# Optimization experiments

Measured on AMD Instinct MI355X. Metric: run time of the kernel, lower is better.

The kernel has to match this reference:

```python
import jax, jax.numpy as jnp
import numpy as np

L, D = 1024, 256
NDIR, NL = 6, 2
H, P, N, K = 8, 64, 32, 4          # nheads, headdim, d_state, d_conv
DI = 2 * D                          # d_inner = expand * d_model
DIN = 2 * DI + 2 * N + H            # in_proj output width (z, xBC, dt)
CONV_DIM = DI + 2 * N               # channels going through depthwise conv
ORDERS = [(0, 1, 2), (0, 2, 1), (1, 0, 2), (1, 2, 0), (2, 0, 1), (2, 1, 0)]  # XYT,XTY,YXT,YTX,TXY,TYX


def setup_inputs() -> dict:
    ks = jax.random.split(jax.random.key(0), 12)
    s = 0.02
    f32 = jnp.float32
    return {
        "vectors": jax.random.normal(ks[0], (L, D), f32),
        "event_coords": jax.random.randint(ks[1], (L, 4), 0, 64, jnp.int32),
        "ln_g": jnp.ones((NDIR, NL, D), f32),
        "ln_b": jnp.zeros((NDIR, NL, D), f32),
        "Win": jax.random.normal(ks[2], (NDIR, NL, D, DIN), f32) * s,
        "conv_w": jax.random.normal(ks[3], (NDIR, NL, CONV_DIM, K), f32) * s,
        "conv_b": jnp.zeros((NDIR, NL, CONV_DIM), f32),
        "dt_bias": jax.random.normal(ks[4], (NDIR, NL, H), f32) * 0.5,
        "A_log": jnp.log(jax.random.uniform(ks[5], (NDIR, NL, H), f32, 1.0, 16.0)),
        "Dp": jnp.ones((NDIR, NL, H), f32),
        "rms_g": jnp.ones((NDIR, NL, DI), f32),
        "Wout": jax.random.normal(ks[6], (NDIR, NL, DI, D), f32) * s,
        "fuse_ln_g": jnp.ones((NDIR * D,), f32),
        "fuse_ln_b": jnp.zeros((NDIR * D,), f32),
        "fuse_W": jax.random.normal(ks[7], (NDIR * D, D), f32) * s,
        "fuse_b": jnp.zeros((D,), f32),
    }


def _layernorm(x, g, b, eps=1e-5):
    mu = jnp.mean(x, -1, keepdims=True)
    var = jnp.mean((x - mu) ** 2, -1, keepdims=True)
    return (x - mu) * jax.lax.rsqrt(var + eps) * g + b


def _causal_dwconv(x, w, b):
    # x: [Bt,L,C]; w: [C,K]. Torch depthwise conv1d with padding K-1, truncated to L.
    k = w.shape[1]
    Lx = x.shape[1]
    xp = jnp.pad(x, ((0, 0), (k - 1, 0), (0, 0)))
    return sum(xp[:, j:j + Lx, :] * w[:, j] for j in range(k)) + b


def _mamba2(x, Win, conv_w, conv_b, dt_bias, A_log, Dp, rms_g, Wout):
    # x: [Bt,L,D] -> [Bt,L,D]. Mamba2 with ngroups=1, rmsnorm gating, no proj biases.
    Bt, Lx, _ = x.shape
    zxbcdt = x @ Win
    z = zxbcdt[..., :DI]
    xBC = zxbcdt[..., DI:DI + CONV_DIM]
    dt = jax.nn.softplus(zxbcdt[..., -H:] + dt_bias)              # [Bt,L,H]
    xBC = jax.nn.silu(_causal_dwconv(xBC, conv_w, conv_b))
    xs = xBC[..., :DI].reshape(Bt, Lx, H, P)                      # [Bt,L,H,P]
    Bm = xBC[..., DI:DI + N]                                      # [Bt,L,N]
    Cm = xBC[..., DI + N:]                                        # [Bt,L,N]
    dA = jnp.exp(dt * (-jnp.exp(A_log)))                          # [Bt,L,H]
    dBx = jnp.einsum('blh,bln,blhp->blhpn', dt, Bm, xs)

    def step(h, inp):
        dA_t, dBx_t, C_t = inp
        h = dA_t[:, :, None, None] * h + dBx_t                    # [Bt,H,P,N]
        return h, jnp.einsum('bhpn,bn->bhp', h, C_t)

    h0 = jnp.zeros((Bt, H, P, N), x.dtype)
    _, ys = jax.lax.scan(step, h0, (dA.transpose(1, 0, 2),
                                    dBx.transpose(1, 0, 2, 3, 4),
                                    Cm.transpose(1, 0, 2)))
    y = ys.transpose(1, 0, 2, 3) + Dp[:, None] * xs               # [Bt,L,H,P]
    u = y.reshape(Bt, Lx, DI) * jax.nn.silu(z)                    # gated RMSNorm
    u = u * jax.lax.rsqrt(jnp.mean(u * u, -1, keepdims=True) + 1e-5) * rms_g
    return u @ Wout


def _forward(vectors, event_coords, ln_g, ln_b, Win, conv_w, conv_b, dt_bias,
             A_log, Dp, rms_g, Wout, fuse_ln_g, fuse_ln_b, fuse_W, fuse_b):
    v = vectors[None]                                             # [1,L,D]
    outs = []
    for i, axes in enumerate(ORDERS):
        idx = jnp.lexsort(tuple(event_coords[:, a] for a in reversed(axes)))
        x = v[:, idx, :]
        for l in range(NL):
            x = x + _mamba2(_layernorm(x, ln_g[i, l], ln_b[i, l]),
                            Win[i, l], conv_w[i, l], conv_b[i, l], dt_bias[i, l],
                            A_log[i, l], Dp[i, l], rms_g[i, l], Wout[i, l])
        outs.append(x[:, jnp.argsort(idx), :])                    # scatter back
    md = jnp.concatenate(outs, -1)                                # [1,L,6D]
    f = _layernorm(md, fuse_ln_g, fuse_ln_b) @ fuse_W + fuse_b
    return jax.nn.gelu(f, approximate=False)[0]                   # [L,D]


def reference(vectors, event_coords, ln_g, ln_b, Win, conv_w, conv_b, dt_bias,
              A_log, Dp, rms_g, Wout, fuse_ln_g, fuse_ln_b, fuse_W, fuse_b):
    return _forward(vectors, event_coords, ln_g, ln_b, Win, conv_w, conv_b, dt_bias,
                    A_log, Dp, rms_g, Wout, fuse_ln_g, fuse_ln_b, fuse_W, fuse_b)
```

## Files before the change

kernel.cpp:

```cpp
#include <hip/hip_runtime.h>
#include <hip/hip_bf16.h>
#include <cstddef>

#define LL 1024
#define DD0 256
#define NDIR 6
#define NL 2
#define HH 8
#define PP 64
#define NN 32
#define KK 4
#define DI 512
#define DIN 1096
#define CONV_DIM 576

#define QC 32
#define NC 32
#define NCSH 5

__constant__ int c_ord[6][3] = {{0,1,2},{0,2,1},{1,0,2},{1,2,0},{2,0,1},{2,1,0}};

typedef __attribute__((ext_vector_type(8))) short bf16x8;
typedef __attribute__((ext_vector_type(4))) float f32x4;

__device__ inline float blockReduceSum256(float v) {
    __shared__ float sred[4];
#pragma unroll
    for (int off = 1; off < 64; off <<= 1) v += __shfl_xor(v, off);
    int lane = threadIdx.x & 63, w = threadIdx.x >> 6;
    __syncthreads();
    if (lane == 0) sred[w] = v;
    __syncthreads();
    return sred[0] + sred[1] + sred[2] + sred[3];
}

__device__ inline float siluf(float x) { return x / (1.f + expf(-x)); }

__device__ inline unsigned short bf16_rn(float x) {
    unsigned u = __float_as_uint(x);
    unsigned r = (u + 0x7fffu + ((u >> 16) & 1u)) >> 16;
    return (unsigned short)r;
}
__device__ inline float bf16_to_f(unsigned short h) {
    return __uint_as_float(((unsigned)h) << 16);
}

__global__ __launch_bounds__(1024)
void sort_kernel(const int* __restrict__ coords, int* __restrict__ perm, int* __restrict__ rank) {
    int q = blockIdx.x, d = blockIdx.y;
    int tid = threadIdx.x;
    __shared__ unsigned keys[LL];
    __shared__ unsigned short part[256][5];
    int a0 = c_ord[d][0], a1 = c_ord[d][1], a2 = c_ord[d][2];
    {
        unsigned c0 = (unsigned)coords[tid*4 + a0];
        unsigned c1 = (unsigned)coords[tid*4 + a1];
        unsigned c2 = (unsigned)coords[tid*4 + a2];
        keys[tid] = (c0 << 22) | (c1 << 16) | (c2 << 10) | (unsigned)tid;
    }
    __syncthreads();
    int il = tid >> 2, jq = tid & 3;
    int i = q*256 + il;
    unsigned ki = keys[i];
    int r = 0;
    int j0 = jq*256;
#pragma unroll 8
    for (int j = j0; j < j0 + 256; ++j) r += (keys[j] < ki) ? 1 : 0;
    part[il][jq] = (unsigned short)r;
    __syncthreads();
    if (tid < 256) {
        int i2 = q*256 + tid;
        int rr = part[tid][0] + part[tid][1] + part[tid][2] + part[tid][3];
        perm[d*LL + rr] = i2;
        rank[d*LL + i2] = rr;
    }
}

__global__ __launch_bounds__(256)
void gather_ln(const float* __restrict__ vectors, const int* __restrict__ perm,
               float* __restrict__ x, unsigned short* __restrict__ Yh,
               unsigned short* __restrict__ Yl,
               const float* __restrict__ g, const float* __restrict__ b) {
    int t = blockIdx.x, d = blockIdx.y, c = threadIdx.x;
    int src = perm[d*LL + t];
    float xv = vectors[(size_t)src*DD0 + c];
    x[((size_t)d*LL + t)*DD0 + c] = xv;
    float s = blockReduceSum256(xv);
    float s2 = blockReduceSum256(xv*xv);
    float mu = s / DD0;
    float var = s2 / DD0 - mu*mu;
    float inv = rsqrtf(var + 1e-5f);
    const float* gr = g + (size_t)d*NL*DD0;
    const float* br = b + (size_t)d*NL*DD0;
    float yv = (xv - mu) * inv * gr[c] + br[c];
    unsigned short h = bf16_rn(yv);
    Yh[((size_t)d*LL + t)*DD0 + c] = h;
    Yl[((size_t)d*LL + t)*DD0 + c] = bf16_rn(yv - bf16_to_f(h));
}

__global__ __launch_bounds__(256)
void ln_split(const float* __restrict__ X, unsigned short* __restrict__ Yh,
              unsigned short* __restrict__ Yl,
              const float* __restrict__ g, const float* __restrict__ b,
              int dd, int rowsPerDir, int gstride) {
    int t = blockIdx.x, d = blockIdx.y;
    const float* xr = X + ((size_t)d*rowsPerDir + t)*dd;
    unsigned short* yh = Yh + ((size_t)d*rowsPerDir + t)*dd;
    unsigned short* yl = Yl + ((size_t)d*rowsPerDir + t)*dd;
    const float* gr = g + (size_t)d*gstride;
    const float* br = b + (size_t)d*gstride;
    float v[6];
    float s = 0.f, s2 = 0.f;
    int cnt = 0;
    for (int c = threadIdx.x; c < dd; c += 256) {
        float xv = xr[c];
        v[cnt++] = xv;
        s += xv; s2 += xv*xv;
    }
    float tot = blockReduceSum256(s);
    float tot2 = blockReduceSum256(s2);
    float mu = tot / dd;
    float var = tot2 / dd - mu*mu;
    float inv = rsqrtf(var + 1e-5f);
    cnt = 0;
    for (int c = threadIdx.x; c < dd; c += 256) {
        float yv = (v[cnt++] - mu) * inv * gr[c] + br[c];
        unsigned short h = bf16_rn(yv);
        yh[c] = h;
        yl[c] = bf16_rn(yv - bf16_to_f(h));
    }
}

__global__ __launch_bounds__(256)
void ln_concat(const float* __restrict__ x, const int* __restrict__ rank,
               unsigned short* __restrict__ Yh, unsigned short* __restrict__ Yl,
               const float* __restrict__ g, const float* __restrict__ b) {
    int t = blockIdx.x, tid = threadIdx.x;
    float v[NDIR];
    float s = 0.f, s2 = 0.f;
#pragma unroll
    for (int d = 0; d < NDIR; ++d) {
        int r = rank[d*LL + t];
        float xv = x[((size_t)d*LL + r)*DD0 + tid];
        v[d] = xv;
        s += xv; s2 += xv*xv;
    }
    float tot = blockReduceSum256(s);
    float tot2 = blockReduceSum256(s2);
    const int dd = NDIR*DD0;
    float mu = tot / dd;
    float var = tot2 / dd - mu*mu;
    float inv = rsqrtf(var + 1e-5f);
#pragma unroll
    for (int d = 0; d < NDIR; ++d) {
        int c = d*DD0 + tid;
        float yv = (v[d] - mu) * inv * g[c] + b[c];
        unsigned short h = bf16_rn(yv);
        Yh[(size_t)t*dd + c] = h;
        Yl[(size_t)t*dd + c] = bf16_rn(yv - bf16_to_f(h));
    }
}

__global__ __launch_bounds__(256)
void tsplit_kernel(const float* __restrict__ W, unsigned short* __restrict__ Th,
                   unsigned short* __restrict__ Tl, int Kd, int Nd) {
    __shared__ float tile[32][33];
    int j0 = blockIdx.x * 32;
    int i0 = blockIdx.y * 32;
    int c = threadIdx.x & 31, r8 = threadIdx.x >> 5;
    const float* Wz = W + (size_t)blockIdx.z * Kd * Nd;
    unsigned short* Thz = Th + (size_t)blockIdx.z * Nd * Kd;
    unsigned short* Tlz = Tl + (size_t)blockIdx.z * Nd * Kd;
#pragma unroll
    for (int s = 0; s < 4; ++s) {
        int i = i0 + r8 + s*8;
        tile[r8 + s*8][c] = (i < Kd && (j0 + c) < Nd) ? Wz[(size_t)i*Nd + j0 + c] : 0.f;
    }
    __syncthreads();
#pragma unroll
    for (int s = 0; s < 4; ++s) {
        int j = j0 + r8 + s*8;
        int i = i0 + c;
        if (j < Nd && i < Kd) {
            float xv = tile[c][r8 + s*8];
            unsigned short h = bf16_rn(xv);
            Thz[(size_t)j*Kd + i] = h;
            Tlz[(size_t)j*Kd + i] = bf16_rn(xv - bf16_to_f(h));
        }
    }
}

template<int MODE, int BM>
__global__ __launch_bounds__(256)
void mfma_gemm(const unsigned short* __restrict__ Ahg, const unsigned short* __restrict__ Alg,
               const unsigned short* __restrict__ Bhg, const unsigned short* __restrict__ Blg,
               float* __restrict__ Cg, int N, int K,
               size_t sA, size_t sB, size_t sC, const float* __restrict__ bias,
               int ksplit) {
    constexpr int MF = BM / 32;
    __shared__ unsigned short AhS[2][BM][40];
    __shared__ unsigned short AlS[2][BM][40];
    __shared__ unsigned short BhS[2][64][40];
    __shared__ unsigned short BlS[2][64][40];
    const unsigned short* Azh = Ahg + (MODE == 3 ? 0 : (size_t)blockIdx.z * sA);
    const unsigned short* Azl = Alg + (MODE == 3 ? 0 : (size_t)blockIdx.z * sA);
    const unsigned short* Bzh = Bhg + (MODE == 3 ? 0 : (size_t)blockIdx.z * sB);
    const unsigned short* Bzl = Blg + (MODE == 3 ? 0 : (size_t)blockIdx.z * sB);
    float* Cz = Cg + (size_t)blockIdx.z * sC;
    int row0 = blockIdx.y * BM;
    int col0 = blockIdx.x * 64;
    int tid = threadIdx.x;
    int lane = tid & 63, wid = tid >> 6;
    int mbase = (wid >> 1) * (BM/2), nbase = (wid & 1) * 32;
    int lr = lane & 15, lk = (lane >> 4) * 8;

    int ar0 = tid >> 2;
    int ar1 = 64 + (tid >> 2);
    int ac  = (tid & 3) * 8;
    int brow = tid >> 2;
    int bc8 = (tid & 3) * 8;
    bool bvalid = (col0 + brow) < N;
    const uint4 z4 = {0u,0u,0u,0u};

    f32x4 acc[MF][2];
#pragma unroll
    for (int m = 0; m < MF; ++m)
#pragma unroll
        for (int n = 0; n < 2; ++n) acc[m][n] = (f32x4){0.f, 0.f, 0.f, 0.f};

    uint4 s0a0, s0a1, s0l0, s0l1, s0bh, s0bl;
    uint4 s1a0, s1a1, s1l0, s1l1, s1bh, s1bl;

#define LOAD_TILE(Ra0,Ra1,Rl0,Rl1,Rbh,Rbl,kt) do {                          \
        size_t ka = (size_t)(kt) * 32;                                       \
        size_t g0 = (size_t)(row0 + ar0)*K + ka + ac;                        \
        Ra0 = *(const uint4*)(Azh + g0);                                     \
        Rl0 = *(const uint4*)(Azl + g0);                                     \
        if (BM == 128) {                                                     \
            size_t g1 = (size_t)(row0 + ar1)*K + ka + ac;                    \
            Ra1 = *(const uint4*)(Azh + g1);                                 \
            Rl1 = *(const uint4*)(Azl + g1);                                 \
        }                                                                    \
        if (bvalid) {                                                        \
            size_t gb = (size_t)(col0 + brow)*K + ka + bc8;                  \
            Rbh = *(const uint4*)(Bzh + gb);                                 \
            Rbl = *(const uint4*)(Bzl + gb);                                 \
        } else { Rbh = z4; Rbl = z4; }                                       \
    } while (0)

#define WRITE_TILE(buf,Ra0,Ra1,Rl0,Rl1,Rbh,Rbl) do {                         \
        *(uint4*)&AhS[buf][ar0][ac] = Ra0;                                   \
        *(uint4*)&AlS[buf][ar0][ac] = Rl0;                                   \
        if (BM == 128) {                                                     \
            *(uint4*)&AhS[buf][ar1 & (BM-1)][ac] = Ra1;                      \
            *(uint4*)&AlS[buf][ar1 & (BM-1)][ac] = Rl1;                      \
        }                                                                    \
        *(uint4*)&BhS[buf][brow][bc8] = Rbh;                                 \
        *(uint4*)&BlS[buf][brow][bc8] = Rbl;                                 \
    } while (0)

#define COMPUTE(buf) do {                                                    \
        bf16x8 afh[MF], afl[MF], bfh[2], bfl[2];                             \
        _Pragma("unroll")                                                    \
        for (int mf = 0; mf < MF; ++mf) {                                    \
            afh[mf] = *(const bf16x8*)&AhS[buf][mbase + mf*16 + lr][lk];     \
            afl[mf] = *(const bf16x8*)&AlS[buf][mbase + mf*16 + lr][lk];     \
        }                                                                    \
        _Pragma("unroll")                                                    \
        for (int nf = 0; nf < 2; ++nf) {                                     \
            bfh[nf] = *(const bf16x8*)&BhS[buf][nbase + nf*16 + lr][lk];     \
            bfl[nf] = *(const bf16x8*)&BlS[buf][nbase + nf*16 + lr][lk];     \
        }                                                                    \
        _Pragma("unroll")                                                    \
        for (int mf = 0; mf < MF; ++mf)                                      \
            _Pragma("unroll")                                                \
            for (int nf = 0; nf < 2; ++nf) {                                 \
                acc[mf][nf] = __builtin_amdgcn_mfma_f32_16x16x32_bf16(afh[mf], bfh[nf], acc[mf][nf], 0, 0, 0); \
                acc[mf][nf] = __builtin_amdgcn_mfma_f32_16x16x32_bf16(afh[mf], bfl[nf], acc[mf][nf], 0, 0, 0); \
                acc[mf][nf] = __builtin_amdgcn_mfma_f32_16x16x32_bf16(afl[mf], bfh[nf], acc[mf][nf], 0, 0, 0); \
            }                                                                \
    } while (0)

    int nt, kt0;
    if (MODE == 3) { nt = ksplit; kt0 = (int)blockIdx.z * ksplit; }
    else           { nt = K >> 5; kt0 = 0; }

    LOAD_TILE(s0a0, s0a1, s0l0, s0l1, s0bh, s0bl, kt0 + 0);
    LOAD_TILE(s1a0, s1a1, s1l0, s1l1, s1bh, s1bl, kt0 + 1);
    WRITE_TILE(0, s0a0, s0a1, s0l0, s0l1, s0bh, s0bl);
    __syncthreads();

    for (int t = 0; t < nt; t += 2) {
        if (t + 2 < nt) LOAD_TILE(s0a0, s0a1, s0l0, s0l1, s0bh, s0bl, kt0 + t + 2);
        COMPUTE(0);
        WRITE_TILE(1, s1a0, s1a1, s1l0, s1l1, s1bh, s1bl);
        __syncthreads();
        if (t + 3 < nt) LOAD_TILE(s1a0, s1a1, s1l0, s1l1, s1bh, s1bl, kt0 + t + 3);
        COMPUTE(1);
        if (t + 2 < nt) WRITE_TILE(0, s0a0, s0a1, s0l0, s0l1, s0bh, s0bl);
        __syncthreads();
    }

#undef LOAD_TILE
#undef WRITE_TILE
#undef COMPUTE

    int crb = (lane >> 4) * 4;
    int cco = lane & 15;
#pragma unroll
    for (int mf = 0; mf < MF; ++mf) {
#pragma unroll
        for (int nf = 0; nf < 2; ++nf) {
            int col = col0 + nbase + nf*16 + cco;
            if (col < N) {
#pragma unroll
                for (int r = 0; r < 4; ++r) {
                    int row = row0 + mbase + mf*16 + crb + r;
                    size_t o = (size_t)row*N + col;
                    float vv = acc[mf][nf][r];
                    if (MODE == 0 || MODE == 3) Cz[o] = vv;
                    else if (MODE == 1) Cz[o] += vv;
                    else {
                        vv += bias[col];
                        Cz[o] = 0.5f * vv * (1.f + erff(vv * 0.70710678118654752f));
                    }
                }
            }
        }
    }
}

__global__ __launch_bounds__(256)
void reduce_gelu(const float* __restrict__ pbuf, const float* __restrict__ bias,
                 float* __restrict__ out) {
    int t = blockIdx.x, c = threadIdx.x;
    size_t o = (size_t)t*DD0 + c;
    const size_t st = (size_t)LL*DD0;
    float v = pbuf[o] + pbuf[o + st] + pbuf[o + 2*st] + pbuf[o + 3*st] + bias[c];
    out[o] = 0.5f * v * (1.f + erff(v * 0.70710678118654752f));
}

__global__ __launch_bounds__(256)
void conv_scan1(const float* __restrict__ zx, const float* __restrict__ conv_w,
                const float* __restrict__ conv_b, const float* __restrict__ dt_bias,
                const float* __restrict__ A_log, const float* __restrict__ Dp,
                float* __restrict__ ys, float* __restrict__ Cbuf,
                float* __restrict__ cstate, float* __restrict__ cumdec, int layer) {
    int bid = blockIdx.x;
    int c = bid & (NC - 1);
    int hd = bid >> NCSH;
    int d = hd >> 3, h = hd & 7;
    int tid = threadIdx.x;
    int t0 = c * QC;

    __shared__ float sxc[QC][132];
    __shared__ float sdt[QC];
    __shared__ float sdA[QC];

    const float* Z = zx + (size_t)d*LL*DIN;

    {
        int col = tid & 127;
        int half = tid >> 7;
        int tstart = t0 + half*16;
        int realc = (col < 64) ? (h*PP + col) : ((col < 96) ? (DI + (col-64)) : (DI + NN + (col-96)));
        int zxcol = DI + realc;
        const float* wr = conv_w + ((size_t)(d*NL + layer)*CONV_DIM + realc)*KK;
        float w0 = wr[0], w1 = wr[1], w2 = wr[2], w3 = wr[3];
        float bias = conv_b[(size_t)(d*NL + layer)*CONV_DIM + realc];
        float z0 = (tstart-3 >= 0) ? Z[(size_t)(tstart-3)*DIN + zxcol] : 0.f;
        float z1 = (tstart-2 >= 0) ? Z[(size_t)(tstart-2)*DIN + zxcol] : 0.f;
        float z2 = (tstart-1 >= 0) ? Z[(size_t)(tstart-1)*DIN + zxcol] : 0.f;
#pragma unroll
        for (int tt = 0; tt < 16; ++tt) {
            int t = tstart + tt;
            float z3 = Z[(size_t)t*DIN + zxcol];
            float acc = bias;
            acc = fmaf(z0, w0, acc);
            acc = fmaf(z1, w1, acc);
            acc = fmaf(z2, w2, acc);
            acc = fmaf(z3, w3, acc);
            sxc[half*16 + tt][col] = siluf(acc);
            z0 = z1; z1 = z2; z2 = z3;
        }
    }
    if (tid < QC) {
        int t = t0 + tid;
        float v = Z[(size_t)t*DIN + (DIN - HH) + h] + dt_bias[(d*NL + layer)*HH + h];
        float sp = (v > 20.f) ? v : log1pf(expf(v));
        sdt[tid] = sp;
        sdA[tid] = expf(-expf(A_log[(d*NL + layer)*HH + h]) * sp);
    }
    __syncthreads();

    int p = tid >> 2, g = tid & 3, n0 = g << 3;
    float dpv = Dp[(d*NL + layer)*HH + h];
    float* ysd = ys + (size_t)d*LL*DI + h*PP + p;
    float* cdd = cumdec + (size_t)d*LL*HH + h;
    float* Cbd = Cbuf + (size_t)d*LL*NN;

    float hs[8];
#pragma unroll
    for (int j = 0; j < 8; ++j) hs[j] = 0.f;
    float cum = 1.f;

    for (int tt = 0; tt < QC; ++tt) {
        float dtv = sdt[tt], dAv = sdA[tt];
        float xv = sxc[tt][p];
        float dtx = dtv * xv;
        float4 b0 = *(const float4*)&sxc[tt][64 + n0];
        float4 b1 = *(const float4*)&sxc[tt][64 + n0 + 4];
        float4 c0 = *(const float4*)&sxc[tt][96 + n0];
        float4 c1 = *(const float4*)&sxc[tt][96 + n0 + 4];
        float B[8] = {b0.x,b0.y,b0.z,b0.w,b1.x,b1.y,b1.z,b1.w};
        float Cv[8] = {c0.x,c0.y,c0.z,c0.w,c1.x,c1.y,c1.z,c1.w};
        float acc = 0.f;
#pragma unroll
        for (int j = 0; j < 8; ++j) {
            hs[j] = fmaf(dAv, hs[j], dtx * B[j]);
            acc = fmaf(hs[j], Cv[j], acc);
        }
        acc += __shfl_xor(acc, 1);
        acc += __shfl_xor(acc, 2);
        int t = t0 + tt;
        if (g == 0) ysd[(size_t)t*DI] = acc + dpv * xv;
        else if (g == 2 && h == 0 && p < NN) Cbd[(size_t)t*NN + p] = sxc[tt][96 + p];
        cum *= dAv;
        if (tid == 0) cdd[(size_t)t*HH] = cum;
    }

    float* cs = cstate + (((size_t)(d*NC + c)*HH + h)*PP + p)*NN + n0;
    float4 s0 = {hs[0], hs[1], hs[2], hs[3]};
    float4 s1 = {hs[4], hs[5], hs[6], hs[7]};
    *(float4*)cs = s0;
    *(float4*)(cs + 4) = s1;
}

__global__ __launch_bounds__(256)
void scan_pass2(float* __restrict__ cstate, const float* __restrict__ cumdec) {
    int hd = blockIdx.x;
    int d = hd >> 3, h = hd & 7;
    int tid = threadIdx.x;
    int p = tid >> 2, g = tid & 3, n0 = g << 3;
    float carry[8];
#pragma unroll
    for (int j = 0; j < 8; ++j) carry[j] = 0.f;
    for (int c = 0; c < NC; ++c) {
        float* cs = cstate + (((size_t)(d*NC + c)*HH + h)*PP + p)*NN + n0;
        float4 s0 = *(const float4*)cs;
        float4 s1 = *(const float4*)(cs + 4);
        float4 w0 = {carry[0], carry[1], carry[2], carry[3]};
        float4 w1 = {carry[4], carry[5], carry[6], carry[7]};
        *(float4*)cs = w0;
        *(float4*)(cs + 4) = w1;
        float dec = cumdec[((size_t)d*LL + (c*QC + QC - 1))*HH + h];
        float s[8] = {s0.x,s0.y,s0.z,s0.w,s1.x,s1.y,s1.z,s1.w};
#pragma unroll
        for (int j = 0; j < 8; ++j) carry[j] = fmaf(dec, carry[j], s[j]);
    }
}

__global__ __launch_bounds__(256)
void scan_pass3(const float* __restrict__ Cbuf, const float* __restrict__ cumdec,
                const float* __restrict__ cstate, float* __restrict__ ys) {
    int bid = blockIdx.x;
    int c = bid & (NC - 1);
    if (c == 0) return;
    int hd = bid >> NCSH;
    int d = hd >> 3, h = hd & 7;
    int tid = threadIdx.x;
    int p = tid >> 2, g = tid & 3, n0 = g << 3;
    int t0 = c * QC;

    __shared__ float scd[QC];
    if (tid < QC) scd[tid] = cumdec[((size_t)d*LL + t0 + tid)*HH + h];

    const float* cs = cstate + (((size_t)(d*NC + c)*HH + h)*PP + p)*NN + n0;
    float4 h0 = *(const float4*)cs;
    float4 h1 = *(const float4*)(cs + 4);
    float hi[8] = {h0.x,h0.y,h0.z,h0.w,h1.x,h1.y,h1.z,h1.w};
    __syncthreads();

    const float* Cbd = Cbuf + (size_t)d*LL*NN;
    float* ysd = ys + (size_t)d*LL*DI + h*PP + p;

    for (int tt = 0; tt < QC; ++tt) {
        int t = t0 + tt;
        const float* row = Cbd + (size_t)t*NN;
        float4 c0 = *(const float4*)(row + n0);
        float4 c1 = *(const float4*)(row + n0 + 4);
        float Cv[8] = {c0.x,c0.y,c0.z,c0.w,c1.x,c1.y,c1.z,c1.w};
        float acc = 0.f;
#pragma unroll
        for (int j = 0; j < 8; ++j) acc = fmaf(hi[j], Cv[j], acc);
        acc += __shfl_xor(acc, 1);
        acc += __shfl_xor(acc, 2);
        if (g == 0) ysd[(size_t)t*DI] += scd[tt] * acc;
    }
}

__global__ __launch_bounds__(256)
void gate_rms(const float* __restrict__ ys, const float* __restrict__ zx,
              const float* __restrict__ rms_g, unsigned short* __restrict__ uh,
              unsigned short* __restrict__ ul, int layer) {
    int t = blockIdx.x, d = blockIdx.y;
    const float* ysr = ys + ((size_t)d*LL + t)*DI;
    const float* zr = zx + ((size_t)d*LL + t)*DIN;
    const float* rg = rms_g + (size_t)(d*NL + layer)*DI;
    unsigned short* uhr = uh + ((size_t)d*LL + t)*DI;
    unsigned short* ulr = ul + ((size_t)d*LL + t)*DI;
    int c2 = threadIdx.x * 2;
    float2 yv = *(const float2*)(ysr + c2);
    float2 zv = *(const float2*)(zr + c2);
    float u0 = yv.x * siluf(zv.x);
    float u1 = yv.y * siluf(zv.y);
    float ss = u0*u0 + u1*u1;
    float tot = blockReduceSum256(ss);
    float scale = rsqrtf(tot / DI + 1e-5f);
    float2 rgv = *(const float2*)(rg + c2);
    float o0 = u0 * scale * rgv.x;
    float o1 = u1 * scale * rgv.y;
    unsigned short h0 = bf16_rn(o0), h1 = bf16_rn(o1);
    unsigned short l0 = bf16_rn(o0 - bf16_to_f(h0)), l1 = bf16_rn(o1 - bf16_to_f(h1));
    *(unsigned*)(uhr + c2) = (unsigned)h0 | ((unsigned)h1 << 16);
    *(unsigned*)(ulr + c2) = (unsigned)l0 | ((unsigned)l1 << 16);
}

extern "C" void kernel_launch(void* const* d_in, const int* in_sizes, int n_in,
                              void* d_out, int out_size, void* d_ws, size_t ws_size,
                              hipStream_t stream) {
    const float* vectors   = (const float*)d_in[0];
    const int*   coords    = (const int*)d_in[1];
    const float* ln_g      = (const float*)d_in[2];
    const float* ln_b      = (const float*)d_in[3];
    const float* Win       = (const float*)d_in[4];
    const float* conv_w    = (const float*)d_in[5];
    const float* conv_b    = (const float*)d_in[6];
    const float* dt_bias   = (const float*)d_in[7];
    const float* A_log     = (const float*)d_in[8];
    const float* Dp        = (const float*)d_in[9];
    const float* rms_g     = (const float*)d_in[10];
    const float* Wout      = (const float*)d_in[11];
    const float* fuse_ln_g = (const float*)d_in[12];
    const float* fuse_ln_b = (const float*)d_in[13];
    const float* fuse_W    = (const float*)d_in[14];
    const float* fuse_b    = (const float*)d_in[15];
    float* out = (float*)d_out;

    char* ws = (char*)d_ws;
    size_t off = 0;
    auto alloc = [&](size_t bytes) -> void* {
        void* p = ws + off;
        off += (bytes + 255) & ~(size_t)255;
        return p;
    };
    int* perm  = (int*)alloc((size_t)NDIR*LL*4);
    int* rank  = (int*)alloc((size_t)NDIR*LL*4);
    float* x   = (float*)alloc((size_t)NDIR*LL*DD0*4);
    unsigned short* xnh = (unsigned short*)alloc((size_t)NDIR*LL*DD0*2);
    unsigned short* xnl = (unsigned short*)alloc((size_t)NDIR*LL*DD0*2);
    float* zx  = (float*)alloc((size_t)NDIR*LL*DIN*4);
    float* Cbuf= (float*)alloc((size_t)NDIR*LL*NN*4);
    float* ysb = (float*)alloc((size_t)NDIR*LL*DI*4);
    unsigned short* uh = (unsigned short*)alloc((size_t)NDIR*LL*DI*2);
    unsigned short* ul = (unsigned short*)alloc((size_t)NDIR*LL*DI*2);
    float* cstate = (float*)alloc((size_t)NDIR*NC*HH*PP*NN*4);
    float* cumdec = (float*)alloc((size_t)NDIR*LL*HH*4);
    float* pbuf  = (float*)alloc((size_t)4*LL*DD0*4);
    unsigned short* WinTh  = (unsigned short*)alloc((size_t)NDIR*NL*DIN*DD0*2);
    unsigned short* WinTl  = (unsigned short*)alloc((size_t)NDIR*NL*DIN*DD0*2);
    unsigned short* WoutTh = (unsigned short*)alloc((size_t)NDIR*NL*DD0*DI*2);
    unsigned short* WoutTl = (unsigned short*)alloc((size_t)NDIR*NL*DD0*DI*2);
    unsigned short* fWTh   = (unsigned short*)alloc((size_t)DD0*(NDIR*DD0)*2);
    unsigned short* fWTl   = (unsigned short*)alloc((size_t)DD0*(NDIR*DD0)*2);
    unsigned short* mdnh = uh;
    unsigned short* mdnl = ul;
    (void)ws_size;

    sort_kernel<<<dim3(4, NDIR), 1024, 0, stream>>>(coords, perm, rank);

    tsplit_kernel<<<dim3((DIN+31)/32, DD0/32, NDIR*NL), 256, 0, stream>>>(Win, WinTh, WinTl, DD0, DIN);
    tsplit_kernel<<<dim3(DD0/32, DI/32, NDIR*NL), 256, 0, stream>>>(Wout, WoutTh, WoutTl, DI, DD0);
    tsplit_kernel<<<dim3(DD0/32, (NDIR*DD0)/32, 1), 256, 0, stream>>>(fuse_W, fWTh, fWTl, NDIR*DD0, DD0);

    for (int l = 0; l < NL; ++l) {
        if (l == 0)
            gather_ln<<<dim3(LL, NDIR), 256, 0, stream>>>(vectors, perm, x, xnh, xnl, ln_g, ln_b);
        else
            ln_split<<<dim3(LL, NDIR), 256, 0, stream>>>(x, xnh, xnl, ln_g + l*DD0, ln_b + l*DD0,
                                                         DD0, LL, NL*DD0);
        mfma_gemm<0,64><<<dim3((DIN+63)/64, LL/64, NDIR), 256, 0, stream>>>(
            xnh, xnl, WinTh + (size_t)l*DIN*DD0, WinTl + (size_t)l*DIN*DD0, zx,
            DIN, DD0, (size_t)LL*DD0, (size_t)NL*DIN*DD0, (size_t)LL*DIN, nullptr, 0);
        conv_scan1<<<NDIR*HH*NC, 256, 0, stream>>>(zx, conv_w, conv_b, dt_bias, A_log, Dp,
                                                   ysb, Cbuf, cstate, cumdec, l);
        scan_pass2<<<NDIR*HH, 256, 0, stream>>>(cstate, cumdec);
        scan_pass3<<<NDIR*HH*NC, 256, 0, stream>>>(Cbuf, cumdec, cstate, ysb);
        gate_rms<<<dim3(LL, NDIR), 256, 0, stream>>>(ysb, zx, rms_g, uh, ul, l);
        mfma_gemm<1,64><<<dim3(DD0/64, LL/64, NDIR), 256, 0, stream>>>(
            uh, ul, WoutTh + (size_t)l*DD0*DI, WoutTl + (size_t)l*DD0*DI, x,
            DD0, DI, (size_t)LL*DI, (size_t)NL*DD0*DI, (size_t)LL*DD0, nullptr, 0);
    }

    ln_concat<<<LL, 256, 0, stream>>>(x, rank, mdnh, mdnl, fuse_ln_g, fuse_ln_b);
    mfma_gemm<3,64><<<dim3(DD0/64, LL/64, 4), 256, 0, stream>>>(
        mdnh, mdnl, fWTh, fWTl, pbuf, DD0, NDIR*DD0, 0, 0, (size_t)LL*DD0, nullptr, 12);
    reduce_gelu<<<LL, 256, 0, stream>>>(pbuf, fuse_b, out);
}
```

Before: 276.8 us.

## Load GEMM B operand directly into registers and merge weight-split kernels

The MFMA GEMM no longer stages the B (weight) tile through shared memory. Each lane loads its bf16x8 B fragments straight from global memory into registers, double-buffered, and feeds them to the MFMAs, which halves LDS traffic and footprint. The three weight transpose/split launches are merged into one kernel with a flattened block index, saving launch overhead. The cost is that B global loads are no longer shared across the two waves that read the same columns, so the same weight data is fetched redundantly through cache.

```diff
diff --git a/kernel.cpp b/kernel.cpp
--- a/kernel.cpp
+++ b/kernel.cpp
@@ -162,15 +162,30 @@
 }
 
 __global__ __launch_bounds__(256)
-void tsplit_kernel(const float* __restrict__ W, unsigned short* __restrict__ Th,
-                   unsigned short* __restrict__ Tl, int Kd, int Nd) {
+void tsplit_all(const float* __restrict__ Wi, const float* __restrict__ Wo,
+                const float* __restrict__ Wf,
+                unsigned short* __restrict__ WinTh, unsigned short* __restrict__ WinTl,
+                unsigned short* __restrict__ WoutTh, unsigned short* __restrict__ WoutTl,
+                unsigned short* __restrict__ fWTh, unsigned short* __restrict__ fWTl) {
+    int bid = blockIdx.x;
+    const float* W; unsigned short *Th, *Tl; int Kd, Nd, bx, by, bz;
+    if (bid < 3360) {
+        int r = bid; W = Wi; Th = WinTh; Tl = WinTl; Kd = DD0; Nd = DIN;
+        bx = r % 35; r /= 35; by = r & 7; bz = r >> 3;
+    } else if (bid < 4896) {
+        int r = bid - 3360; W = Wo; Th = WoutTh; Tl = WoutTl; Kd = DI; Nd = DD0;
+        bx = r & 7; r >>= 3; by = r & 15; bz = r >> 4;
+    } else {
+        int r = bid - 4896; W = Wf; Th = fWTh; Tl = fWTl; Kd = NDIR*DD0; Nd = DD0;
+        bx = r & 7; by = r >> 3; bz = 0;
+    }
     __shared__ float tile[32][33];
-    int j0 = blockIdx.x * 32;
-    int i0 = blockIdx.y * 32;
+    int j0 = bx * 32;
+    int i0 = by * 32;
     int c = threadIdx.x & 31, r8 = threadIdx.x >> 5;
-    const float* Wz = W + (size_t)blockIdx.z * Kd * Nd;
-    unsigned short* Thz = Th + (size_t)blockIdx.z * Nd * Kd;
-    unsigned short* Tlz = Tl + (size_t)blockIdx.z * Nd * Kd;
+    const float* Wz = W + (size_t)bz * Kd * Nd;
+    unsigned short* Thz = Th + (size_t)bz * Nd * Kd;
+    unsigned short* Tlz = Tl + (size_t)bz * Nd * Kd;
 #pragma unroll
     for (int s = 0; s < 4; ++s) {
         int i = i0 + r8 + s*8;
@@ -190,125 +205,120 @@
     }
 }
 
-template<int MODE, int BM>
+template<int MODE>
 __global__ __launch_bounds__(256)
 void mfma_gemm(const unsigned short* __restrict__ Ahg, const unsigned short* __restrict__ Alg,
                const unsigned short* __restrict__ Bhg, const unsigned short* __restrict__ Blg,
                float* __restrict__ Cg, int N, int K,
                size_t sA, size_t sB, size_t sC, const float* __restrict__ bias,
                int ksplit) {
-    constexpr int MF = BM / 32;
-    __shared__ unsigned short AhS[2][BM][40];
-    __shared__ unsigned short AlS[2][BM][40];
-    __shared__ unsigned short BhS[2][64][40];
-    __shared__ unsigned short BlS[2][64][40];
+    __shared__ unsigned short AhS[2][64][40];
+    __shared__ unsigned short AlS[2][64][40];
     const unsigned short* Azh = Ahg + (MODE == 3 ? 0 : (size_t)blockIdx.z * sA);
     const unsigned short* Azl = Alg + (MODE == 3 ? 0 : (size_t)blockIdx.z * sA);
     const unsigned short* Bzh = Bhg + (MODE == 3 ? 0 : (size_t)blockIdx.z * sB);
     const unsigned short* Bzl = Blg + (MODE == 3 ? 0 : (size_t)blockIdx.z * sB);
     float* Cz = Cg + (size_t)blockIdx.z * sC;
-    int row0 = blockIdx.y * BM;
+    int row0 = blockIdx.y * 64;
     int col0 = blockIdx.x * 64;
     int tid = threadIdx.x;
     int lane = tid & 63, wid = tid >> 6;
-    int mbase = (wid >> 1) * (BM/2), nbase = (wid & 1) * 32;
+    int mbase = (wid >> 1) * 32, nbase = (wid & 1) * 32;
     int lr = lane & 15, lk = (lane >> 4) * 8;
 
     int ar0 = tid >> 2;
-    int ar1 = 64 + (tid >> 2);
     int ac  = (tid & 3) * 8;
-    int brow = tid >> 2;
-    int bc8 = (tid & 3) * 8;
-    bool bvalid = (col0 + brow) < N;
+    int bcol0 = col0 + nbase + lr;
+    int bcol1 = col0 + nbase + 16 + lr;
+    bool bok0 = bcol0 < N, bok1 = bcol1 < N;
+    size_t bro0 = (size_t)(bok0 ? bcol0 : 0) * K;
+    size_t bro1 = (size_t)(bok1 ? bcol1 : 0) * K;
     const uint4 z4 = {0u,0u,0u,0u};
 
-    f32x4 acc[MF][2];
-#pragma unroll
-    for (int m = 0; m < MF; ++m)
+    f32x4 acc[2][2];
+#pragma unroll
+    for (int m = 0; m < 2; ++m)
 #pragma unroll
         for (int n = 0; n < 2; ++n) acc[m][n] = (f32x4){0.f, 0.f, 0.f, 0.f};
 
-    uint4 s0a0, s0a1, s0l0, s0l1, s0bh, s0bl;
-    uint4 s1a0, s1a1, s1l0, s1l1, s1bh, s1bl;
-
-#define LOAD_TILE(Ra0,Ra1,Rl0,Rl1,Rbh,Rbl,kt) do {                          \
-        size_t ka = (size_t)(kt) * 32;                                       \
-        size_t g0 = (size_t)(row0 + ar0)*K + ka + ac;                        \
-        Ra0 = *(const uint4*)(Azh + g0);                                     \
-        Rl0 = *(const uint4*)(Azl + g0);                                     \
-        if (BM == 128) {                                                     \
-            size_t g1 = (size_t)(row0 + ar1)*K + ka + ac;                    \
-            Ra1 = *(const uint4*)(Azh + g1);                                 \
-            Rl1 = *(const uint4*)(Azl + g1);                                 \
-        }                                                                    \
-        if (bvalid) {                                                        \
-            size_t gb = (size_t)(col0 + brow)*K + ka + bc8;                  \
-            Rbh = *(const uint4*)(Bzh + gb);                                 \
-            Rbl = *(const uint4*)(Bzl + gb);                                 \
-        } else { Rbh = z4; Rbl = z4; }                                       \
+    uint4 sa0h, sa0l, sa1h, sa1l;
+    uint4 b0h0, b0h1, b0l0, b0l1;
+    uint4 b1h0, b1h1, b1l0, b1l1;
+
+#define LOADA(H,L,kt) do {                                                   \
+        size_t g0 = (size_t)(row0 + ar0)*K + (size_t)(kt)*32 + ac;           \
+        H = *(const uint4*)(Azh + g0);                                       \
+        L = *(const uint4*)(Azl + g0);                                       \
     } while (0)
 
-#define WRITE_TILE(buf,Ra0,Ra1,Rl0,Rl1,Rbh,Rbl) do {                         \
-        *(uint4*)&AhS[buf][ar0][ac] = Ra0;                                   \
-        *(uint4*)&AlS[buf][ar0][ac] = Rl0;                                   \
-        if (BM == 128) {                                                     \
-            *(uint4*)&AhS[buf][ar1 & (BM-1)][ac] = Ra1;                      \
-            *(uint4*)&AlS[buf][ar1 & (BM-1)][ac] = Rl1;                      \
-        }                                                                    \
-        *(uint4*)&BhS[buf][brow][bc8] = Rbh;                                 \
-        *(uint4*)&BlS[buf][brow][bc8] = Rbl;                                 \
+#define WRITEA(buf,H,L) do {                                                 \
+        *(uint4*)&AhS[buf][ar0][ac] = H;                                     \
+        *(uint4*)&AlS[buf][ar0][ac] = L;                                     \
     } while (0)
 
-#define COMPUTE(buf) do {                                                    \
-        bf16x8 afh[MF], afl[MF], bfh[2], bfl[2];                             \
+#define LOADB(H0,H1,L0,L1,kt) do {                                           \
+        size_t ko = (size_t)(kt)*32 + lk;                                    \
+        H0 = bok0 ? *(const uint4*)(Bzh + bro0 + ko) : z4;                   \
+        L0 = bok0 ? *(const uint4*)(Bzl + bro0 + ko) : z4;                   \
+        H1 = bok1 ? *(const uint4*)(Bzh + bro1 + ko) : z4;                   \
+        L1 = bok1 ? *(const uint4*)(Bzl + bro1 + ko) : z4;                   \
+    } while (0)
+
+#define COMPUTE(buf,H0,H1,L0,L1) do {                                        \
+        bf16x8 afh[2], afl[2];                                               \
         _Pragma("unroll")                                                    \
-        for (int mf = 0; mf < MF; ++mf) {                                    \
+        for (int mf = 0; mf < 2; ++mf) {                                     \
             afh[mf] = *(const bf16x8*)&AhS[buf][mbase + mf*16 + lr][lk];     \
             afl[mf] = *(const bf16x8*)&AlS[buf][mbase + mf*16 + lr][lk];     \
         }                                                                    \
+        bf16x8 BH0 = __builtin_bit_cast(bf16x8, H0);                         \
+        bf16x8 BH1 = __builtin_bit_cast(bf16x8, H1);                         \
+        bf16x8 BL0 = __builtin_bit_cast(bf16x8, L0);                         \
+        bf16x8 BL1 = __builtin_bit_cast(bf16x8, L1);                         \
         _Pragma("unroll")                                                    \
-        for (int nf = 0; nf < 2; ++nf) {                                     \
-            bfh[nf] = *(const bf16x8*)&BhS[buf][nbase + nf*16 + lr][lk];     \
-            bfl[nf] = *(const bf16x8*)&BlS[buf][nbase + nf*16 + lr][lk];     \
+        for (int mf = 0; mf < 2; ++mf) {                                     \
+            acc[mf][0] = __builtin_amdgcn_mfma_f32_16x16x32_bf16(afh[mf], BH0, acc[mf][0], 0, 0, 0); \
+            acc[mf][0] = __builtin_amdgcn_mfma_f32_16x16x32_bf16(afh[mf], BL0, acc[mf][0], 0, 0, 0); \
+            acc[mf][0] = __builtin_amdgcn_mfma_f32_16x16x32_bf16(afl[mf], BH0, acc[mf][0], 0, 0, 0); \
+            acc[mf][1] = __builtin_amdgcn_mfma_f32_16x16x32_bf16(afh[mf], BH1, acc[mf][1], 0, 0, 0); \
+            acc[mf][1] = __builtin_amdgcn_mfma_f32_16x16x32_bf16(afh[mf], BL1, acc[mf][1], 0, 0, 0); \
+            acc[mf][1] = __builtin_amdgcn_mfma_f32_16x16x32_bf16(afl[mf], BH1, acc[mf][1], 0, 0, 0); \
         }                                                                    \
-        _Pragma("unroll")                                                    \
-        for (int mf = 0; mf < MF; ++mf)                                      \
-            _Pragma("unroll")                                                \
-            for (int nf = 0; nf < 2; ++nf) {                                 \
-                acc[mf][nf] = __builtin_amdgcn_mfma_f32_16x16x32_bf16(afh[mf], bfh[nf], acc[mf][nf], 0, 0, 0); \
-                acc[mf][nf] = __builtin_amdgcn_mfma_f32_16x16x32_bf16(afh[mf], bfl[nf], acc[mf][nf], 0, 0, 0); \
-                acc[mf][nf] = __builtin_amdgcn_mfma_f32_16x16x32_bf16(afl[mf], bfh[nf], acc[mf][nf], 0, 0, 0); \
-            }                                                                \
     } while (0)
 
     int nt, kt0;
     if (MODE == 3) { nt = ksplit; kt0 = (int)blockIdx.z * ksplit; }
     else           { nt = K >> 5; kt0 = 0; }
 
-    LOAD_TILE(s0a0, s0a1, s0l0, s0l1, s0bh, s0bl, kt0 + 0);
-    LOAD_TILE(s1a0, s1a1, s1l0, s1l1, s1bh, s1bl, kt0 + 1);
-    WRITE_TILE(0, s0a0, s0a1, s0l0, s0l1, s0bh, s0bl);
+    LOADA(sa0h, sa0l, kt0 + 0);
+    LOADA(sa1h, sa1l, kt0 + 1);
+    LOADB(b0h0, b0h1, b0l0, b0l1, kt0 + 0);
+    LOADB(b1h0, b1h1, b1l0, b1l1, kt0 + 1);
+    WRITEA(0, sa0h, sa0l);
     __syncthreads();
 
     for (int t = 0; t < nt; t += 2) {
-        if (t + 2 < nt) LOAD_TILE(s0a0, s0a1, s0l0, s0l1, s0bh, s0bl, kt0 + t + 2);
-        COMPUTE(0);
-        WRITE_TILE(1, s1a0, s1a1, s1l0, s1l1, s1bh, s1bl);
+        if (t + 2 < nt) LOADA(sa0h, sa0l, kt0 + t + 2);
+        COMPUTE(0, b0h0, b0h1, b0l0, b0l1);
+        if (t + 2 < nt) LOADB(b0h0, b0h1, b0l0, b0l1, kt0 + t + 2);
+        WRITEA(1, sa1h, sa1l);
         __syncthreads();
-        if (t + 3 < nt) LOAD_TILE(s1a0, s1a1, s1l0, s1l1, s1bh, s1bl, kt0 + t + 3);
-        COMPUTE(1);
-        if (t + 2 < nt) WRITE_TILE(0, s0a0, s0a1, s0l0, s0l1, s0bh, s0bl);
+        if (t + 3 < nt) LOADA(sa1h, sa1l, kt0 + t + 3);
+        COMPUTE(1, b1h0, b1h1, b1l0, b1l1);
+        if (t + 3 < nt) LOADB(b1h0, b1h1, b1l0, b1l1, kt0 + t + 3);
+        if (t + 2 < nt) WRITEA(0, sa0h, sa0l);
         __syncthreads();
     }
 
-#undef LOAD_TILE
-#undef WRITE_TILE
+#undef LOADA
+#undef WRITEA
+#undef LOADB
 #undef COMPUTE
 
     int crb = (lane >> 4) * 4;
     int cco = lane & 15;
 #pragma unroll
-    for (int mf = 0; mf < MF; ++mf) {
+    for (int mf = 0; mf < 2; ++mf) {
 #pragma unroll
         for (int nf = 0; nf < 2; ++nf) {
             int col = col0 + nbase + nf*16 + cco;
@@ -579,9 +589,8 @@
 
     sort_kernel<<<dim3(4, NDIR), 1024, 0, stream>>>(coords, perm, rank);
 
-    tsplit_kernel<<<dim3((DIN+31)/32, DD0/32, NDIR*NL), 256, 0, stream>>>(Win, WinTh, WinTl, DD0, DIN);
-    tsplit_kernel<<<dim3(DD0/32, DI/32, NDIR*NL), 256, 0, stream>>>(Wout, WoutTh, WoutTl, DI, DD0);
-    tsplit_kernel<<<dim3(DD0/32, (NDIR*DD0)/32, 1), 256, 0, stream>>>(fuse_W, fWTh, fWTl, NDIR*DD0, DD0);
+    tsplit_all<<<5280, 256, 0, stream>>>(Win, Wout, fuse_W,
+                                         WinTh, WinTl, WoutTh, WoutTl, fWTh, fWTl);
 
     for (int l = 0; l < NL; ++l) {
         if (l == 0)
@@ -589,7 +598,7 @@
         else
             ln_split<<<dim3(LL, NDIR), 256, 0, stream>>>(x, xnh, xnl, ln_g + l*DD0, ln_b + l*DD0,
                                                          DD0, LL, NL*DD0);
-        mfma_gemm<0,64><<<dim3((DIN+63)/64, LL/64, NDIR), 256, 0, stream>>>(
+        mfma_gemm<0><<<dim3((DIN+63)/64, LL/64, NDIR), 256, 0, stream>>>(
             xnh, xnl, WinTh + (size_t)l*DIN*DD0, WinTl + (size_t)l*DIN*DD0, zx,
             DIN, DD0, (size_t)LL*DD0, (size_t)NL*DIN*DD0, (size_t)LL*DIN, nullptr, 0);
         conv_scan1<<<NDIR*HH*NC, 256, 0, stream>>>(zx, conv_w, conv_b, dt_bias, A_log, Dp,
@@ -597,13 +606,13 @@
         scan_pass2<<<NDIR*HH, 256, 0, stream>>>(cstate, cumdec);
         scan_pass3<<<NDIR*HH*NC, 256, 0, stream>>>(Cbuf, cumdec, cstate, ysb);
         gate_rms<<<dim3(LL, NDIR), 256, 0, stream>>>(ysb, zx, rms_g, uh, ul, l);
-        mfma_gemm<1,64><<<dim3(DD0/64, LL/64, NDIR), 256, 0, stream>>>(
+        mfma_gemm<1><<<dim3(DD0/64, LL/64, NDIR), 256, 0, stream>>>(
             uh, ul, WoutTh + (size_t)l*DD0*DI, WoutTl + (size_t)l*DD0*DI, x,
             DD0, DI, (size_t)LL*DI, (size_t)NL*DD0*DI, (size_t)LL*DD0, nullptr, 0);
     }
 
     ln_concat<<<LL, 256, 0, stream>>>(x, rank, mdnh, mdnl, fuse_ln_g, fuse_ln_b);
-    mfma_gemm<3,64><<<dim3(DD0/64, LL/64, 4), 256, 0, stream>>>(
+    mfma_gemm<3><<<dim3(DD0/64, LL/64, 4), 256, 0, stream>>>(
         mdnh, mdnl, fWTh, fWTl, pbuf, DD0, NDIR*DD0, 0, 0, (size_t)LL*DD0, nullptr, 12);
     reduce_gelu<<<LL, 256, 0, stream>>>(pbuf, fuse_b, out);
 }
```

New measurement: 310.8 us. 1.12x slower.
